# Kernel optimization log

Hardware: AMD Instinct MI355X
Metric: run time of the kernel (lower is better)

Reference implementation:

```python
import jax, jax.numpy as jnp
import numpy as np


def ste_sign(x):
    # larq ste_sign forward: sign(x) with sign(0) = 1
    return jnp.where(x >= 0, 1.0, -1.0).astype(x.dtype)


def setup_inputs() -> dict:
    key = jax.random.key(0)
    ks = jax.random.split(key, 8)
    B, H, W, Cin, Cout = 32, 56, 56, 256, 256
    x = jax.random.normal(ks[0], (B, H, W, Cin), dtype=jnp.float32)
    bias1 = jax.random.normal(ks[1], (1, 1, 1, Cin), dtype=jnp.float32) * 0.01
    kernel = jax.random.normal(ks[2], (3, 3, Cin, Cout), dtype=jnp.float32) * 0.1
    # BatchNormalization(scale=False): beta learnable, gamma=1, moving stats
    bn_beta = jax.random.normal(ks[3], (Cout,), dtype=jnp.float32) * 0.01
    bn_mean = jax.random.normal(ks[4], (Cout,), dtype=jnp.float32) * 0.01
    bn_var = jax.random.uniform(ks[5], (Cout,), dtype=jnp.float32, minval=0.5, maxval=1.5)
    bias2 = jax.random.normal(ks[6], (1, 1, 1, Cout), dtype=jnp.float32) * 0.01
    return {"x": x, "bias1": bias1, "kernel": kernel, "bn_beta": bn_beta,
            "bn_mean": bn_mean, "bn_var": bn_var, "bias2": bias2}


def reference(x, bias1, kernel, bn_beta, bn_mean, bn_var, bias2):
    eps = 1e-3  # keras BatchNormalization default epsilon
    strides = 1
    # lb_activation_1: learnable bias + ste_sign activation
    a = ste_sign(x + bias1)
    # QuantConv2D: binarize kernel, 'same' padding conv (NHWC, HWIO)
    qk = ste_sign(kernel)
    y = jax.lax.conv_general_dilated(
        a, qk, window_strides=(strides, strides), padding='SAME',
        dimension_numbers=('NHWC', 'HWIO', 'NHWC'))
    # BatchNormalization(scale=False) inference: (y - mean)/sqrt(var+eps) + beta
    y = (y - bn_mean) * jax.lax.rsqrt(bn_var + eps) + bn_beta
    # strides == 1: no avgpool residual branch
    # lb_activation_2: learnable bias + relu
    out = jax.nn.relu(y + bias2)
    return out
```

## Files before the change

### kernel.cpp

```cpp
#include <hip/hip_runtime.h>


typedef int v4i __attribute__((ext_vector_type(4)));
typedef unsigned int u32;

#define NB   32
#define HW   56
#define HP   58
#define HP2  (HP*HP)
#define CIN  256
#define COUT 256
#define NPIX (NB*HW*HW)
#define KTOT 2304
#define BM   128
#define BN   128
#define NSTEP 18
#define NWG  ((NPIX/BM)*(COUT/BN))

#define PA_BYTES ((size_t)NB*HP*HP*CIN)
#define WT_OFF   PA_BYTES
#define WT_BYTES ((size_t)KTOT*COUT)
#define SC_OFF   (WT_OFF + WT_BYTES)
#define SH_OFF   (SC_OFF + 1024)

__device__ __forceinline__ void g2l16(const void* g, void* l) {
    __builtin_amdgcn_global_load_lds(
        (const __attribute__((address_space(1))) void*)g,
        (__attribute__((address_space(3))) void*)l, 16, 0, 0);
}

__global__ __launch_bounds__(256) void pack_a_kernel(
    const float* __restrict__ x, const float* __restrict__ b1,
    signed char* __restrict__ pa)
{
    const int lane = threadIdx.x & 63;
    const int pp = blockIdx.x * 4 + (threadIdx.x >> 6);
    const int n = pp / HP2, r = pp % HP2, ph = r / HP, pw = r % HP;
    const int ci = lane * 4;
    u32 o = 0;
    if (ph >= 1 && ph <= HW && pw >= 1 && pw <= HW) {
        const int pix = (n * HW + ph - 1) * HW + (pw - 1);
        const float4 xv = *(const float4*)(x + (size_t)pix * CIN + ci);
        const float4 bv = *(const float4*)(b1 + ci);
        o  = (u32)(unsigned char)((xv.x + bv.x >= 0.f) ? 1 : -1);
        o |= (u32)(unsigned char)((xv.y + bv.y >= 0.f) ? 1 : -1) << 8;
        o |= (u32)(unsigned char)((xv.z + bv.z >= 0.f) ? 1 : -1) << 16;
        o |= (u32)(unsigned char)((xv.w + bv.w >= 0.f) ? 1 : -1) << 24;
    }
    *(u32*)(pa + (size_t)pp * CIN + ci) = o;
}

__global__ __launch_bounds__(256) void packw_kernel(
    const float* __restrict__ k, signed char* __restrict__ wt)
{
    __shared__ signed char tile[64][256];
    const int t = threadIdx.x, k0 = blockIdx.x * 64;
    for (int j = 0; j < 64; ++j)
        tile[j][t] = (k[(size_t)(k0 + j) * COUT + t] >= 0.f) ? 1 : -1;
    __syncthreads();
    u32 wd[16];
#pragma unroll
    for (int j = 0; j < 16; ++j) wd[j] = 0;
#pragma unroll
    for (int j = 0; j < 64; ++j)
        wd[j >> 2] |= ((u32)(unsigned char)tile[j][t]) << ((j & 3) * 8);
    uint4* dst = (uint4*)(wt + (size_t)t * KTOT + k0);
#pragma unroll
    for (int j = 0; j < 4; ++j)
        dst[j] = make_uint4(wd[4*j], wd[4*j+1], wd[4*j+2], wd[4*j+3]);
}

__global__ __launch_bounds__(256) void bnprep_kernel(
    const float* __restrict__ beta, const float* __restrict__ mean,
    const float* __restrict__ var, const float* __restrict__ b2,
    float* __restrict__ scale, float* __restrict__ shift)
{
    const int t = threadIdx.x;
    const float s = rsqrtf(var[t] + 1e-3f);
    scale[t] = s;
    shift[t] = beta[t] - mean[t] * s + b2[t];
}

__global__ __launch_bounds__(256, 2) void conv_mfma_kernel(
    const signed char* __restrict__ pa, const signed char* __restrict__ wt,
    const float* __restrict__ scale, const float* __restrict__ shift,
    float* __restrict__ out)
{
    __shared__ signed char L[2][32768];

    const int t = threadIdx.x, l = t & 63, v = t >> 6;
    const int vm = v >> 1, vn = v & 1;
    const int swz  = (blockIdx.x & 7) * (NWG / 8) + (blockIdx.x >> 3);
    const int tile = swz >> 1;
    const int co0  = (swz & 1) << 7;
    const int p0 = tile * BM;

    const signed char* abase[2];
#pragma unroll
    for (int i = 0; i < 2; ++i) {
        const int q = (t >> 2) + i * 64;
        const int p = p0 + q;
        const int n = p / 3136, r = p % 3136, h = r / 56, w = r % 56;
        const int aswz = (((t & 3) ^ ((q >> 1) & 3)) << 4);
        abase[i] = pa + ((size_t)(n * HP + h) * HP + w) * CIN + aswz;
    }
    const signed char* wbase[2];
#pragma unroll
    for (int j = 0; j < 2; ++j) {
        const int r = j * 64 + (t >> 2);
        const int bswz = (((t & 3) ^ ((r >> 1) & 3)) << 4);
        wbase[j] = wt + (size_t)(co0 + r) * KTOT + bswz;
    }

    int aoff[4], boff[4];
#pragma unroll
    for (int pg = 0; pg < 4; ++pg) {
        const int row = vm * 64 + pg * 16 + (l & 15);
        aoff[pg] = row * 64 + ((((l >> 4) ^ (row >> 1)) & 3) << 4);
    }
#pragma unroll
    for (int cg = 0; cg < 4; ++cg) {
        const int row = vn * 64 + cg * 16 + (l & 15);
        boff[cg] = 16384 + row * 64 + ((((l >> 4) ^ (row >> 1)) & 3) << 4);
    }

    v4i acc[4][4];
#pragma unroll
    for (int i = 0; i < 4; ++i)
#pragma unroll
        for (int j = 0; j < 4; ++j) acc[i][j] = (v4i){0, 0, 0, 0};

    auto goffA = [&](int k64) {
        const int tap = k64 >> 2, cq = k64 & 3;
        const int ty = tap / 3, tx = tap - ty * 3;
        return ((ty * HP + tx) << 8) + (cq << 6);
    };
    auto STAGE = [&](int buf, int s) {
#pragma unroll
        for (int ks = 0; ks < 2; ++ks) {
            const int k64 = 2 * s + ks;
            const int go = goffA(k64);
            g2l16(abase[0] + go, &L[buf][ks * 8192 + v * 1024]);
            g2l16(abase[1] + go, &L[buf][ks * 8192 + 4096 + v * 1024]);
            g2l16(wbase[0] + (k64 << 6), &L[buf][16384 + ks * 8192 + v * 1024]);
            g2l16(wbase[1] + (k64 << 6), &L[buf][16384 + ks * 8192 + 4096 + v * 1024]);
        }
    };

    STAGE(0, 0);
    asm volatile("s_waitcnt vmcnt(0)" ::: "memory");
    __builtin_amdgcn_s_barrier();

#pragma unroll 1
    for (int s = 0; s < NSTEP; ++s) {
        const int cur = s & 1, nxt = cur ^ 1;
        const signed char* Lc = &L[cur][0];
        if (s + 1 < NSTEP) STAGE(nxt, s + 1);
        v4i af[2][4], bf[2][4];
#pragma unroll
        for (int ks = 0; ks < 2; ++ks) {
#pragma unroll
            for (int pg = 0; pg < 4; ++pg)
                af[ks][pg] = *(const v4i*)(Lc + ks * 8192 + aoff[pg]);
#pragma unroll
            for (int cg = 0; cg < 4; ++cg)
                bf[ks][cg] = *(const v4i*)(Lc + ks * 8192 + boff[cg]);
        }
        __builtin_amdgcn_s_setprio(1);
#pragma unroll
        for (int ks = 0; ks < 2; ++ks)
#pragma unroll
            for (int pg = 0; pg < 4; ++pg)
#pragma unroll
                for (int cg = 0; cg < 4; ++cg)
                    acc[pg][cg] = __builtin_amdgcn_mfma_i32_16x16x64_i8(
                        af[ks][pg], bf[ks][cg], acc[pg][cg], 0, 0, 0);
        __builtin_amdgcn_s_setprio(0);
        asm volatile("s_waitcnt vmcnt(0)" ::: "memory");
        __builtin_amdgcn_s_barrier();
    }

#pragma unroll
    for (int cg = 0; cg < 4; ++cg) {
        const int co = co0 + vn * 64 + cg * 16 + (l & 15);
        const float sc = scale[co], sh = shift[co];
#pragma unroll
        for (int pg = 0; pg < 4; ++pg) {
            const int prow0 = p0 + vm * 64 + pg * 16 + (l >> 4) * 4;
#pragma unroll
            for (int rr = 0; rr < 4; ++rr) {
                const float y = (float)acc[pg][cg][rr];
                out[(size_t)(prow0 + rr) * COUT + co] = fmaxf(fmaf(y, sc, sh), 0.f);
            }
        }
    }
}

extern "C" void kernel_launch(void* const* d_in, const int* in_sizes, int n_in,
                              void* d_out, int out_size, void* d_ws, size_t ws_size,
                              hipStream_t stream)
{
    const float* x      = (const float*)d_in[0];
    const float* bias1  = (const float*)d_in[1];
    const float* kernel = (const float*)d_in[2];
    const float* bn_beta = (const float*)d_in[3];
    const float* bn_mean = (const float*)d_in[4];
    const float* bn_var  = (const float*)d_in[5];
    const float* bias2   = (const float*)d_in[6];
    float* out = (float*)d_out;

    signed char* pa  = (signed char*)d_ws;
    signed char* wtp = (signed char*)d_ws + WT_OFF;
    float* scale = (float*)((char*)d_ws + SC_OFF);
    float* shift = (float*)((char*)d_ws + SH_OFF);

    pack_a_kernel<<<dim3(NB * HP2 / 4), dim3(256), 0, stream>>>(x, bias1, pa);
    packw_kernel<<<dim3(KTOT / 64), dim3(256), 0, stream>>>(kernel, wtp);
    bnprep_kernel<<<dim3(1), dim3(256), 0, stream>>>(bn_beta, bn_mean, bn_var, bias2,
                                                     scale, shift);
    conv_mfma_kernel<<<dim3(NWG), dim3(256), 0, stream>>>(pa, wtp, scale, shift, out);
}
```

Baseline: 102.9 us.

## Load binarized weights directly from global in MFMA fragment layout, halve LDS

Weights are repacked into an MFMA-fragment-ordered layout so each lane fetches its B operand with a single 16-byte global load instead of staging through LDS. LDS per block drops to half, only activations remain double-buffered in shared memory. This removes LDS write/read traffic and barrier-covered staging for weights. The cost is that weight loads now sit on the critical path before the MFMAs with no prefetch, and each block re-reads weights from L2/global.

```diff
diff --git a/kernel.cpp b/kernel.cpp
--- a/kernel.cpp
+++ b/kernel.cpp
@@ -51,7 +51,7 @@
 }
 
 __global__ __launch_bounds__(256) void packw_kernel(
-    const float* __restrict__ k, signed char* __restrict__ wt)
+    const float* __restrict__ k, signed char* __restrict__ wf)
 {
     __shared__ signed char tile[64][256];
     const int t = threadIdx.x, k0 = blockIdx.x * 64;
@@ -64,10 +64,10 @@
 #pragma unroll
     for (int j = 0; j < 64; ++j)
         wd[j >> 2] |= ((u32)(unsigned char)tile[j][t]) << ((j & 3) * 8);
-    uint4* dst = (uint4*)(wt + (size_t)t * KTOT + k0);
-#pragma unroll
-    for (int j = 0; j < 4; ++j)
-        dst[j] = make_uint4(wd[4*j], wd[4*j+1], wd[4*j+2], wd[4*j+3]);
+#pragma unroll
+    for (int c = 0; c < 4; ++c)
+        *(uint4*)(wf + (((size_t)blockIdx.x * 4 + c) * 256 + t) * 16) =
+            make_uint4(wd[4*c], wd[4*c+1], wd[4*c+2], wd[4*c+3]);
 }
 
 __global__ __launch_bounds__(256) void bnprep_kernel(
@@ -82,11 +82,11 @@
 }
 
 __global__ __launch_bounds__(256, 2) void conv_mfma_kernel(
-    const signed char* __restrict__ pa, const signed char* __restrict__ wt,
+    const signed char* __restrict__ pa, const signed char* __restrict__ wf,
     const float* __restrict__ scale, const float* __restrict__ shift,
     float* __restrict__ out)
 {
-    __shared__ signed char L[2][32768];
+    __shared__ signed char L[2][16384];
 
     const int t = threadIdx.x, l = t & 63, v = t >> 6;
     const int vm = v >> 1, vn = v & 1;
@@ -104,24 +104,18 @@
         const int aswz = (((t & 3) ^ ((q >> 1) & 3)) << 4);
         abase[i] = pa + ((size_t)(n * HP + h) * HP + w) * CIN + aswz;
     }
-    const signed char* wbase[2];
-#pragma unroll
-    for (int j = 0; j < 2; ++j) {
-        const int r = j * 64 + (t >> 2);
-        const int bswz = (((t & 3) ^ ((r >> 1) & 3)) << 4);
-        wbase[j] = wt + (size_t)(co0 + r) * KTOT + bswz;
-    }
-
-    int aoff[4], boff[4];
+
+    int aoff[4];
 #pragma unroll
     for (int pg = 0; pg < 4; ++pg) {
         const int row = vm * 64 + pg * 16 + (l & 15);
         aoff[pg] = row * 64 + ((((l >> 4) ^ (row >> 1)) & 3) << 4);
     }
+    u32 boffg[4];
 #pragma unroll
     for (int cg = 0; cg < 4; ++cg) {
-        const int row = vn * 64 + cg * 16 + (l & 15);
-        boff[cg] = 16384 + row * 64 + ((((l >> 4) ^ (row >> 1)) & 3) << 4);
+        const int co = co0 + vn * 64 + cg * 16 + (l & 15);
+        boffg[cg] = (u32)((((l >> 4) * 256) + co) * 16);
     }
 
     v4i acc[4][4];
@@ -142,8 +136,6 @@
             const int go = goffA(k64);
             g2l16(abase[0] + go, &L[buf][ks * 8192 + v * 1024]);
             g2l16(abase[1] + go, &L[buf][ks * 8192 + 4096 + v * 1024]);
-            g2l16(wbase[0] + (k64 << 6), &L[buf][16384 + ks * 8192 + v * 1024]);
-            g2l16(wbase[1] + (k64 << 6), &L[buf][16384 + ks * 8192 + 4096 + v * 1024]);
         }
     };
 
@@ -159,12 +151,13 @@
         v4i af[2][4], bf[2][4];
 #pragma unroll
         for (int ks = 0; ks < 2; ++ks) {
+            const u32 kbase = (u32)(2 * s + ks) * 16384;
+#pragma unroll
+            for (int cg = 0; cg < 4; ++cg)
+                bf[ks][cg] = *(const v4i*)(wf + kbase + boffg[cg]);
 #pragma unroll
             for (int pg = 0; pg < 4; ++pg)
                 af[ks][pg] = *(const v4i*)(Lc + ks * 8192 + aoff[pg]);
-#pragma unroll
-            for (int cg = 0; cg < 4; ++cg)
-                bf[ks][cg] = *(const v4i*)(Lc + ks * 8192 + boff[cg]);
         }
         __builtin_amdgcn_s_setprio(1);
 #pragma unroll
@@ -210,13 +203,13 @@
     float* out = (float*)d_out;
 
     signed char* pa  = (signed char*)d_ws;
-    signed char* wtp = (signed char*)d_ws + WT_OFF;
+    signed char* wfp = (signed char*)d_ws + WT_OFF;
     float* scale = (float*)((char*)d_ws + SC_OFF);
     float* shift = (float*)((char*)d_ws + SH_OFF);
 
     pack_a_kernel<<<dim3(NB * HP2 / 4), dim3(256), 0, stream>>>(x, bias1, pa);
-    packw_kernel<<<dim3(KTOT / 64), dim3(256), 0, stream>>>(kernel, wtp);
+    packw_kernel<<<dim3(KTOT / 64), dim3(256), 0, stream>>>(kernel, wfp);
     bnprep_kernel<<<dim3(1), dim3(256), 0, stream>>>(bn_beta, bn_mean, bn_var, bias2,
                                                      scale, shift);
-    conv_mfma_kernel<<<dim3(NWG), dim3(256), 0, stream>>>(pa, wtp, scale, shift, out);
-}
+    conv_mfma_kernel<<<dim3(NWG), dim3(256), 0, stream>>>(pa, wfp, scale, shift, out);
+}
```

New measurement: 99.10 us, median of 3. -3.7%, faster.
